# Kernel optimization log

Hardware: AMD Instinct MI355X
Metric: run time of the kernel (lower is better)

The kernel has to match this reference:

```python
import jax, jax.numpy as jnp
import numpy as np

B, N = 16, 286
EMB_DIM = 4
CLOUD_DIM = 4
NB = 3          # number_of_basis
HID = 150       # radial MLP hidden width
RADIUS = 3.0    # neighbor radius / max_radius of cosine basis
FF = 512


def sp5(x):
    # torch Softplus(beta=5)
    return jax.nn.softplus(5.0 * x) / 5.0


def cosine_basis(r):
    # e3nn CosineBasisModel embedding: cos^2 bumps on [0, RADIUS]
    centers = jnp.linspace(0.0, RADIUS, NB)
    step = centers[1] - centers[0]
    d = (r[..., None] - centers) / step                     # [B,N,N,NB]
    return jnp.cos(jnp.pi / 2 * d) ** 2 * (jnp.abs(d) < 1.0)


def cloud_conv(feats, dist, mask, ws, bs, dim_out):
    # radial MLP on pairwise distances -> per-pair [dim_out, dim_in] kernel (l=0 only)
    x = cosine_basis(dist)
    for w, b in zip(ws[:-1], bs[:-1]):
        x = sp5(x @ w + b)
    R = x @ ws[-1] + bs[-1]                                 # [B,N,N,dim_out*dim_in]
    b_, n_ = dist.shape[0], dist.shape[1]
    k = R.reshape(b_, n_, n_, dim_out, -1) * mask[..., None, None]
    nb = jnp.maximum(mask.sum(-1), 1.0)                     # neighbors per atom [B,N]
    out = jnp.einsum('zabij,zbj->zai', k, feats) / jnp.sqrt(nb)[..., None]
    return out


def setup_inputs() -> dict:
    key = jax.random.key(0)
    ks = jax.random.split(key, 32)
    xyz = jax.random.normal(ks[0], (B, N, 3), dtype=jnp.float32)
    Z = jax.random.randint(ks[1], (B, N), 0, 11)
    emb = jax.random.normal(ks[2], (11, EMB_DIM), dtype=jnp.float32)
    inp = {'xyz': xyz, 'Z': Z, 'emb': emb}
    # radial MLPs per cloud: 3 -> 150 -> 150 -> 150 -> dim_out*dim_in (=16)
    dims = [NB, HID, HID, HID, CLOUD_DIM * CLOUD_DIM]
    ki = 3
    for c in range(2):
        for l in range(4):
            w = jax.random.normal(ks[ki], (dims[l], dims[l + 1]), dtype=jnp.float32) / np.sqrt(dims[l])
            b = jnp.zeros((dims[l + 1],), dtype=jnp.float32)
            inp[f'c{c}_w{l}'] = w
            inp[f'c{c}_b{l}'] = b
            ki += 1
    cloud_out = CLOUD_DIM * 2  # cloud_dim * cloud_order^2 * nclouds = 8
    inp['fc_w'] = jax.random.normal(ks[ki], (cloud_out, FF), dtype=jnp.float32) / np.sqrt(cloud_out); ki += 1
    inp['fc_b'] = jnp.zeros((FF,), dtype=jnp.float32)
    inp['bn_g'] = jnp.ones((FF,), dtype=jnp.float32)
    inp['bn_b'] = jnp.zeros((FF,), dtype=jnp.float32)
    inp['out_w'] = jax.random.normal(ks[ki], (FF, 1), dtype=jnp.float32) / np.sqrt(FF); ki += 1
    inp['out_b'] = jnp.zeros((1,), dtype=jnp.float32)
    return inp


def reference(xyz, Z, emb,
              c0_w0, c0_b0, c0_w1, c0_b1, c0_w2, c0_b2, c0_w3, c0_b3,
              c1_w0, c1_b0, c1_w1, c1_b1, c1_w2, c1_b2, c1_w3, c1_b3,
              fc_w, fc_b, bn_g, bn_b, out_w, out_b):
    feats = emb[Z]                                          # [B,N,emb_dim]
    diff = xyz[:, :, None, :] - xyz[:, None, :, :]
    dist = jnp.sqrt(jnp.sum(diff * diff, -1) + 1e-12)       # [B,N,N]
    mask = (dist < RADIUS).astype(feats.dtype)
    f1 = cloud_conv(feats, dist, mask,
                    [c0_w0, c0_w1, c0_w2, c0_w3], [c0_b0, c0_b1, c0_b2, c0_b3], CLOUD_DIM)
    f2 = cloud_conv(f1, dist, mask,
                    [c1_w0, c1_w1, c1_w2, c1_w3], [c1_b0, c1_b1, c1_b2, c1_b3], CLOUD_DIM)
    feats_cat = jnp.concatenate([f1, f2], axis=2)           # [B,N,8]
    # lp_pool2d(norm=2, kernel=(N,1)) == L2 norm over atom dim
    pooled = jnp.sqrt(jnp.sum(feats_cat ** 2, axis=1))      # [B,8]
    h = jax.nn.softplus(pooled @ fc_w + fc_b)
    mean = h.mean(0)
    var = h.var(0)
    h = jax.nn.softplus((h - mean) / jnp.sqrt(var + 1e-5) * bn_g + bn_b)
    return jax.nn.sigmoid(h @ out_w + out_b)[:, 0]          # [B]
```

## Files before the change

### kernel.cpp

```cpp
#include <hip/hip_runtime.h>
#include <hip/hip_bf16.h>
#include <hip/hip_fp16.h>
#include <math.h>

#define B_SZ   16
#define N_ATOM 286
#define NT     1024
#define HIDW   150
#define FF_DIM 512
#define WPAD   152
#define WROWS  151

__device__ __forceinline__ float softplus_f(float x) {
  return fmaxf(x, 0.0f) + log1pf(expf(-fabsf(x)));
}
__device__ __forceinline__ float sp5_f(float x) {
  float t = 5.0f * x;
  return (fmaxf(t, 0.0f) + log1pf(expf(-fabsf(t)))) * 0.2f;
}

__global__ __launch_bounds__(256) void prep_kernel(
    const float* __restrict__ w1a, const float* __restrict__ b1a,
    const float* __restrict__ w2a, const float* __restrict__ b2a,
    const float* __restrict__ w1c, const float* __restrict__ b1c,
    const float* __restrict__ w2c, const float* __restrict__ b2c,
    float* __restrict__ Wp) {
  const int m = blockIdx.y;
  const float* W  = (m == 0) ? w1a : (m == 1) ? w2a : (m == 2) ? w1c : w2c;
  const float* Bb = (m == 0) ? b1a : (m == 1) ? b2a : (m == 2) ? b1c : b2c;
  int idx = blockIdx.x * 256 + threadIdx.x;
  if (idx < WROWS * WPAD) {
    int i = idx / WPAD, o = idx % WPAD;
    float v = 0.0f;
    if (o < HIDW) v = (i < HIDW) ? W[i * HIDW + o] : Bb[o];
    Wp[(size_t)m * WROWS * WPAD + idx] = v;
  }
}

__device__ __forceinline__ void hidden_layer_v2(
    const float* __restrict__ Wp,
    const float* __restrict__ src,
    float* __restrict__ dst,
    int jj, int e0) {
  const float4 bb = *(const float4*)(Wp + HIDW * WPAD + 4 * jj);
  float4 a0 = bb, a1 = bb;
  #pragma unroll 8
  for (int i = 0; i < HIDW; ++i) {
    float4 wv = *(const float4*)(Wp + i * WPAD + 4 * jj);
    float2 h  = *(const float2*)(src + i * 8 + e0);
    a0.x = __builtin_fmaf(h.x, wv.x, a0.x); a1.x = __builtin_fmaf(h.y, wv.x, a1.x);
    a0.y = __builtin_fmaf(h.x, wv.y, a0.y); a1.y = __builtin_fmaf(h.y, wv.y, a1.y);
    a0.z = __builtin_fmaf(h.x, wv.z, a0.z); a1.z = __builtin_fmaf(h.y, wv.z, a1.z);
    a0.w = __builtin_fmaf(h.x, wv.w, a0.w); a1.w = __builtin_fmaf(h.y, wv.w, a1.w);
  }
  *(float2*)(dst + (4 * jj + 0) * 8 + e0) = make_float2(sp5_f(a0.x), sp5_f(a1.x));
  *(float2*)(dst + (4 * jj + 1) * 8 + e0) = make_float2(sp5_f(a0.y), sp5_f(a1.y));
  *(float2*)(dst + (4 * jj + 2) * 8 + e0) = make_float2(sp5_f(a0.z), sp5_f(a1.z));
  *(float2*)(dst + (4 * jj + 3) * 8 + e0) = make_float2(sp5_f(a0.w), sp5_f(a1.w));
}

__global__ __launch_bounds__(256) void table_kernel(
    const float* __restrict__ a_w0, const float* __restrict__ a_b0,
    const float* __restrict__ a_w3, const float* __restrict__ a_b3,
    const float* __restrict__ c_w0, const float* __restrict__ c_b0,
    const float* __restrict__ c_w3, const float* __restrict__ c_b3,
    const float* __restrict__ Wp,
    __half* __restrict__ tabh0, __half* __restrict__ tabh1) {
  __shared__ float actA[WPAD * 8];
  __shared__ float actB[WPAD * 8];

  const int nblk = NT / 8;
  const int cloud = (blockIdx.x >= nblk) ? 1 : 0;
  const int blk   = blockIdx.x - cloud * nblk;
  const float* w0 = cloud ? c_w0 : a_w0;  const float* b0 = cloud ? c_b0 : a_b0;
  const float* w3 = cloud ? c_w3 : a_w3;  const float* b3 = cloud ? c_b3 : a_b3;
  const float* Wp1 = Wp + (size_t)(cloud * 2)     * WROWS * WPAD;
  const float* Wp2 = Wp + (size_t)(cloud * 2 + 1) * WROWS * WPAD;
  __half* table = cloud ? tabh1 : tabh0;

  const int tid  = threadIdx.x;
  const int lane = tid & 63;
  const int wave = __builtin_amdgcn_readfirstlane(tid >> 6);
  const int e0   = wave * 2;
  const int gbase = blk * 8;
  const int jj = (lane < 38) ? lane : 37;

  float x0[3], x1[3];
  #pragma unroll
  for (int k = 0; k < 3; ++k) {
    float r0 = 3.0f * (float)(gbase + e0)     / (float)(NT - 1);
    float r1 = 3.0f * (float)(gbase + e0 + 1) / (float)(NT - 1);
    float d0 = (r0 - 1.5f * (float)k) * (1.0f / 1.5f);
    float d1 = (r1 - 1.5f * (float)k) * (1.0f / 1.5f);
    float c0 = cosf(1.57079632679489662f * d0);
    float c1 = cosf(1.57079632679489662f * d1);
    x0[k] = (fabsf(d0) < 1.0f) ? c0 * c0 : 0.0f;
    x1[k] = (fabsf(d1) < 1.0f) ? c1 * c1 : 0.0f;
  }

  #pragma unroll
  for (int c = 0; c < 3; ++c) {
    int o = lane + 64 * c;
    int oc = (o < HIDW) ? o : (HIDW - 1);
    float w00 = w0[oc], w01 = w0[HIDW + oc], w02 = w0[2 * HIDW + oc], bb = b0[oc];
    float h0 = sp5_f(bb + x0[0] * w00 + x0[1] * w01 + x0[2] * w02);
    float h1 = sp5_f(bb + x1[0] * w00 + x1[1] * w01 + x1[2] * w02);
    if (o < HIDW) *(float2*)(actA + o * 8 + e0) = make_float2(h0, h1);
  }

  hidden_layer_v2(Wp1, actA, actB, jj, e0);
  hidden_layer_v2(Wp2, actB, actA, jj, e0);

  {
    const int o  = lane & 15;
    const int ig = lane >> 4;
    float a0 = 0.f, a1 = 0.f;
    for (int i = ig; i < HIDW; i += 4) {
      float wv = w3[i * 16 + o];
      float h0 = actA[i * 8 + e0];
      float h1 = actA[i * 8 + e0 + 1];
      a0 = __builtin_fmaf(h0, wv, a0);
      a1 = __builtin_fmaf(h1, wv, a1);
    }
    a0 += __shfl_xor(a0, 16, 64); a0 += __shfl_xor(a0, 32, 64);
    a1 += __shfl_xor(a1, 16, 64); a1 += __shfl_xor(a1, 32, 64);
    if (lane < 16) {
      float bb = b3[o];
      table[(size_t)(gbase + e0)     * 16 + o] = __float2half(a0 + bb);
      table[(size_t)(gbase + e0 + 1) * 16 + o] = __float2half(a1 + bb);
    }
  }
}

__device__ __forceinline__ void cvt8(uint4 q, float* out) {
  const __half2* h = (const __half2*)&q;
  #pragma unroll
  for (int k = 0; k < 4; ++k) {
    float2 f = __half22float2(h[k]);
    out[2 * k] = f.x; out[2 * k + 1] = f.y;
  }
}

__global__ __launch_bounds__(256) void conv_kernel(
    const float* __restrict__ xyz, const int* __restrict__ Z,
    const float* __restrict__ emb, const float* __restrict__ feats_in,
    const __half* __restrict__ tabh, float* __restrict__ f_out, int gather) {
  const int wave = threadIdx.x >> 6;
  const int lane = threadIdx.x & 63;
  const int row = blockIdx.x * 4 + wave;
  if (row >= B_SZ * N_ATOM) return;
  const int z = row / N_ATOM, a = row % N_ATOM;
  const float* xz = xyz + (size_t)z * N_ATOM * 3;
  const float ax = xz[a * 3 + 0], ay = xz[a * 3 + 1], az = xz[a * 3 + 2];

  float acc[4] = {0.f, 0.f, 0.f, 0.f};
  float cnt = 0.f;
  for (int b = lane; b < N_ATOM; b += 64) {
    float bx = xz[b * 3 + 0], by = xz[b * 3 + 1], bz = xz[b * 3 + 2];
    float dx = ax - bx, dy = ay - by, dz = az - bz;
    float r = sqrtf(dx * dx + dy * dy + dz * dz + 1e-12f);
    if (r < 3.0f) {
      cnt += 1.0f;
      float t = r * ((float)(NT - 1) / 3.0f);
      int idx = (int)t;
      if (idx > NT - 2) idx = NT - 2;
      float fr = t - (float)idx;
      const uint4* Tp = (const uint4*)(tabh + (size_t)idx * 16);
      uint4 q0 = Tp[0], q1 = Tp[1], q2 = Tp[2], q3 = Tp[3];
      float4 fb;
      if (gather) {
        int zi = Z[z * N_ATOM + b];
        fb = *(const float4*)(emb + (size_t)zi * 4);
      } else {
        fb = *(const float4*)(feats_in + ((size_t)z * N_ATOM + b) * 4);
      }
      float r0[16], r1[16];
      cvt8(q0, r0); cvt8(q1, r0 + 8);
      cvt8(q2, r1); cvt8(q3, r1 + 8);
      #pragma unroll
      for (int i = 0; i < 4; ++i) {
        float v0 = r0[4 * i + 0] + fr * (r1[4 * i + 0] - r0[4 * i + 0]);
        float v1 = r0[4 * i + 1] + fr * (r1[4 * i + 1] - r0[4 * i + 1]);
        float v2 = r0[4 * i + 2] + fr * (r1[4 * i + 2] - r0[4 * i + 2]);
        float v3 = r0[4 * i + 3] + fr * (r1[4 * i + 3] - r0[4 * i + 3]);
        acc[i] += v0 * fb.x + v1 * fb.y + v2 * fb.z + v3 * fb.w;
      }
    }
  }
  #pragma unroll
  for (int m = 32; m > 0; m >>= 1) {
    #pragma unroll
    for (int i = 0; i < 4; ++i) acc[i] += __shfl_xor(acc[i], m, 64);
    cnt += __shfl_xor(cnt, m, 64);
  }
  if (lane == 0) {
    float nb = cnt < 1.0f ? 1.0f : cnt;
    float sc = 1.0f / sqrtf(nb);
    float4 o;
    o.x = acc[0] * sc; o.y = acc[1] * sc; o.z = acc[2] * sc; o.w = acc[3] * sc;
    *(float4*)(f_out + (size_t)row * 4) = o;
  }
}

__global__ __launch_bounds__(256) void pool_kernel(
    const float* __restrict__ f1, const float* __restrict__ f2,
    float* __restrict__ pool_sq) {
  __shared__ float red[4][8];
  const int z = blockIdx.x;
  const int tid = threadIdx.x;
  const int lane = tid & 63, wave = tid >> 6;
  float s[8] = {0.f, 0.f, 0.f, 0.f, 0.f, 0.f, 0.f, 0.f};
  for (int a = tid; a < N_ATOM; a += 256) {
    float4 v1 = *(const float4*)(f1 + ((size_t)z * N_ATOM + a) * 4);
    float4 v2 = *(const float4*)(f2 + ((size_t)z * N_ATOM + a) * 4);
    s[0] += v1.x * v1.x; s[1] += v1.y * v1.y;
    s[2] += v1.z * v1.z; s[3] += v1.w * v1.w;
    s[4] += v2.x * v2.x; s[5] += v2.y * v2.y;
    s[6] += v2.z * v2.z; s[7] += v2.w * v2.w;
  }
  #pragma unroll
  for (int m = 32; m > 0; m >>= 1) {
    #pragma unroll
    for (int k = 0; k < 8; ++k) s[k] += __shfl_xor(s[k], m, 64);
  }
  if (lane == 0) {
    #pragma unroll
    for (int k = 0; k < 8; ++k) red[wave][k] = s[k];
  }
  __syncthreads();
  if (tid < 8)
    pool_sq[z * 8 + tid] = red[0][tid] + red[1][tid] + red[2][tid] + red[3][tid];
}

__global__ __launch_bounds__(512) void tail_kernel(
    const float* __restrict__ pool_sq,
    const float* __restrict__ fc_w, const float* __restrict__ fc_b,
    const float* __restrict__ bn_g, const float* __restrict__ bn_b,
    const float* __restrict__ out_w, const float* __restrict__ out_b,
    float* __restrict__ out) {
  __shared__ float pooled[16][8];
  __shared__ float part[8][16];
  const int tid = threadIdx.x;

  if (tid < 128) pooled[tid >> 3][tid & 7] = sqrtf(pool_sq[tid]);
  __syncthreads();

  const int f = tid;
  float hv[16];
  float mean = 0.f;
  #pragma unroll
  for (int z = 0; z < 16; ++z) {
    float a = fc_b[f];
    #pragma unroll
    for (int c = 0; c < 8; ++c) a += pooled[z][c] * fc_w[c * FF_DIM + f];
    hv[z] = softplus_f(a);
    mean += hv[z];
  }
  mean *= (1.0f / 16.0f);
  float var = 0.f;
  #pragma unroll
  for (int z = 0; z < 16; ++z) { float d = hv[z] - mean; var += d * d; }
  var *= (1.0f / 16.0f);
  float istd = 1.0f / sqrtf(var + 1e-5f);
  float g = bn_g[f], bb = bn_b[f], ow = out_w[f];
  float contrib[16];
  #pragma unroll
  for (int z = 0; z < 16; ++z)
    contrib[z] = softplus_f((hv[z] - mean) * istd * g + bb) * ow;

  const int lane = tid & 63, wv = tid >> 6;
  #pragma unroll
  for (int m = 32; m > 0; m >>= 1) {
    #pragma unroll
    for (int z = 0; z < 16; ++z) contrib[z] += __shfl_xor(contrib[z], m, 64);
  }
  if (lane == 0) {
    #pragma unroll
    for (int z = 0; z < 16; ++z) part[wv][z] = contrib[z];
  }
  __syncthreads();
  if (tid < 16) {
    float s = out_b[0];
    #pragma unroll
    for (int w8 = 0; w8 < 8; ++w8) s += part[w8][tid];
    out[tid] = 1.0f / (1.0f + expf(-s));
  }
}

extern "C" void kernel_launch(void* const* d_in, const int* in_sizes, int n_in,
                              void* d_out, int out_size, void* d_ws, size_t ws_size,
                              hipStream_t stream) {
  const float* xyz = (const float*)d_in[0];
  const int*   Z   = (const int*)d_in[1];
  const float* emb = (const float*)d_in[2];
  const float* c0[8]; const float* c1[8];
  for (int i = 0; i < 8; ++i) {
    c0[i] = (const float*)d_in[3 + i];
    c1[i] = (const float*)d_in[11 + i];
  }
  const float* fc_w  = (const float*)d_in[19];
  const float* fc_b  = (const float*)d_in[20];
  const float* bn_g  = (const float*)d_in[21];
  const float* bn_b  = (const float*)d_in[22];
  const float* out_w = (const float*)d_in[23];
  const float* out_b = (const float*)d_in[24];
  float* out = (float*)d_out;

  float* wsf = (float*)d_ws;
  float* Wp = wsf;
  float* f1 = Wp + (size_t)4 * WROWS * WPAD;
  float* f2 = f1 + (size_t)B_SZ * N_ATOM * 4;
  float* pool_sq = f2 + (size_t)B_SZ * N_ATOM * 4;
  __half* tabh0 = (__half*)(pool_sq + 128);
  __half* tabh1 = tabh0 + (size_t)NT * 16;

  {
    dim3 g((WROWS * WPAD + 255) / 256, 4);
    prep_kernel<<<g, 256, 0, stream>>>(c0[2], c0[3], c0[4], c0[5],
                                       c1[2], c1[3], c1[4], c1[5], Wp);
  }

  table_kernel<<<2 * (NT / 8), 256, 0, stream>>>(
      c0[0], c0[1], c0[6], c0[7],
      c1[0], c1[1], c1[6], c1[7],
      Wp, tabh0, tabh1);

  const int conv_blocks = (B_SZ * N_ATOM + 3) / 4;
  conv_kernel<<<conv_blocks, 256, 0, stream>>>(xyz, Z, emb, (const float*)nullptr,
                                               tabh0, f1, 1);
  conv_kernel<<<conv_blocks, 256, 0, stream>>>(xyz, Z, emb, f1,
                                               tabh1, f2, 0);

  pool_kernel<<<B_SZ, 256, 0, stream>>>(f1, f2, pool_sq);

  tail_kernel<<<1, 512, 0, stream>>>(pool_sq, fc_w, fc_b, bn_g, bn_b,
                                     out_w, out_b, out);
}
```

Baseline: 183.6 us.

## Stage per-molecule coordinates and features in LDS; branchless masked conv accumulation

Conv blocks are now assigned per molecule (72 blocks per batch element), and each block loads that molecule's coordinates and neighbor features into shared memory once. The per-pair loop reads positions and features from LDS instead of global memory. The radius test becomes a multiplicative mask, so table lookups run for every pair without divergence. The table kernel inlines the hidden-layer routine with restrict pointers and unroll 10. The cost is extra table loads for out-of-radius pairs and an added block-level sync.

```diff
diff --git a/kernel.cpp b/kernel.cpp
--- a/kernel.cpp
+++ b/kernel.cpp
@@ -10,6 +10,7 @@
 #define FF_DIM 512
 #define WPAD   152
 #define WROWS  151
+#define BLK_PER_Z 72
 
 __device__ __forceinline__ float softplus_f(float x) {
   return fmaxf(x, 0.0f) + log1pf(expf(-fabsf(x)));
@@ -37,28 +38,6 @@
   }
 }
 
-__device__ __forceinline__ void hidden_layer_v2(
-    const float* __restrict__ Wp,
-    const float* __restrict__ src,
-    float* __restrict__ dst,
-    int jj, int e0) {
-  const float4 bb = *(const float4*)(Wp + HIDW * WPAD + 4 * jj);
-  float4 a0 = bb, a1 = bb;
-  #pragma unroll 8
-  for (int i = 0; i < HIDW; ++i) {
-    float4 wv = *(const float4*)(Wp + i * WPAD + 4 * jj);
-    float2 h  = *(const float2*)(src + i * 8 + e0);
-    a0.x = __builtin_fmaf(h.x, wv.x, a0.x); a1.x = __builtin_fmaf(h.y, wv.x, a1.x);
-    a0.y = __builtin_fmaf(h.x, wv.y, a0.y); a1.y = __builtin_fmaf(h.y, wv.y, a1.y);
-    a0.z = __builtin_fmaf(h.x, wv.z, a0.z); a1.z = __builtin_fmaf(h.y, wv.z, a1.z);
-    a0.w = __builtin_fmaf(h.x, wv.w, a0.w); a1.w = __builtin_fmaf(h.y, wv.w, a1.w);
-  }
-  *(float2*)(dst + (4 * jj + 0) * 8 + e0) = make_float2(sp5_f(a0.x), sp5_f(a1.x));
-  *(float2*)(dst + (4 * jj + 1) * 8 + e0) = make_float2(sp5_f(a0.y), sp5_f(a1.y));
-  *(float2*)(dst + (4 * jj + 2) * 8 + e0) = make_float2(sp5_f(a0.z), sp5_f(a1.z));
-  *(float2*)(dst + (4 * jj + 3) * 8 + e0) = make_float2(sp5_f(a0.w), sp5_f(a1.w));
-}
-
 __global__ __launch_bounds__(256) void table_kernel(
     const float* __restrict__ a_w0, const float* __restrict__ a_b0,
     const float* __restrict__ a_w3, const float* __restrict__ a_b3,
@@ -74,8 +53,8 @@
   const int blk   = blockIdx.x - cloud * nblk;
   const float* w0 = cloud ? c_w0 : a_w0;  const float* b0 = cloud ? c_b0 : a_b0;
   const float* w3 = cloud ? c_w3 : a_w3;  const float* b3 = cloud ? c_b3 : a_b3;
-  const float* Wp1 = Wp + (size_t)(cloud * 2)     * WROWS * WPAD;
-  const float* Wp2 = Wp + (size_t)(cloud * 2 + 1) * WROWS * WPAD;
+  const float* __restrict__ Wp1 = Wp + (size_t)(cloud * 2)     * WROWS * WPAD;
+  const float* __restrict__ Wp2 = Wp + (size_t)(cloud * 2 + 1) * WROWS * WPAD;
   __half* table = cloud ? tabh1 : tabh0;
 
   const int tid  = threadIdx.x;
@@ -105,11 +84,46 @@
     float w00 = w0[oc], w01 = w0[HIDW + oc], w02 = w0[2 * HIDW + oc], bb = b0[oc];
     float h0 = sp5_f(bb + x0[0] * w00 + x0[1] * w01 + x0[2] * w02);
     float h1 = sp5_f(bb + x1[0] * w00 + x1[1] * w01 + x1[2] * w02);
-    if (o < HIDW) *(float2*)(actA + o * 8 + e0) = make_float2(h0, h1);
-  }
-
-  hidden_layer_v2(Wp1, actA, actB, jj, e0);
-  hidden_layer_v2(Wp2, actB, actA, jj, e0);
+    if (o < HIDW) *(float2*)(&actA[o * 8 + e0]) = make_float2(h0, h1);
+  }
+
+  {
+    const float* __restrict__ Wb = Wp1 + 4 * jj;
+    float4 a0 = *(const float4*)(Wp1 + HIDW * WPAD + 4 * jj);
+    float4 a1 = a0;
+    #pragma unroll 10
+    for (int i = 0; i < HIDW; ++i) {
+      float4 wv = *(const float4*)(Wb + i * WPAD);
+      float2 h  = *(const float2*)(&actA[i * 8 + e0]);
+      a0.x = __builtin_fmaf(h.x, wv.x, a0.x); a1.x = __builtin_fmaf(h.y, wv.x, a1.x);
+      a0.y = __builtin_fmaf(h.x, wv.y, a0.y); a1.y = __builtin_fmaf(h.y, wv.y, a1.y);
+      a0.z = __builtin_fmaf(h.x, wv.z, a0.z); a1.z = __builtin_fmaf(h.y, wv.z, a1.z);
+      a0.w = __builtin_fmaf(h.x, wv.w, a0.w); a1.w = __builtin_fmaf(h.y, wv.w, a1.w);
+    }
+    *(float2*)(&actB[(4 * jj + 0) * 8 + e0]) = make_float2(sp5_f(a0.x), sp5_f(a1.x));
+    *(float2*)(&actB[(4 * jj + 1) * 8 + e0]) = make_float2(sp5_f(a0.y), sp5_f(a1.y));
+    *(float2*)(&actB[(4 * jj + 2) * 8 + e0]) = make_float2(sp5_f(a0.z), sp5_f(a1.z));
+    *(float2*)(&actB[(4 * jj + 3) * 8 + e0]) = make_float2(sp5_f(a0.w), sp5_f(a1.w));
+  }
+
+  {
+    const float* __restrict__ Wb = Wp2 + 4 * jj;
+    float4 a0 = *(const float4*)(Wp2 + HIDW * WPAD + 4 * jj);
+    float4 a1 = a0;
+    #pragma unroll 10
+    for (int i = 0; i < HIDW; ++i) {
+      float4 wv = *(const float4*)(Wb + i * WPAD);
+      float2 h  = *(const float2*)(&actB[i * 8 + e0]);
+      a0.x = __builtin_fmaf(h.x, wv.x, a0.x); a1.x = __builtin_fmaf(h.y, wv.x, a1.x);
+      a0.y = __builtin_fmaf(h.x, wv.y, a0.y); a1.y = __builtin_fmaf(h.y, wv.y, a1.y);
+      a0.z = __builtin_fmaf(h.x, wv.z, a0.z); a1.z = __builtin_fmaf(h.y, wv.z, a1.z);
+      a0.w = __builtin_fmaf(h.x, wv.w, a0.w); a1.w = __builtin_fmaf(h.y, wv.w, a1.w);
+    }
+    *(float2*)(&actA[(4 * jj + 0) * 8 + e0]) = make_float2(sp5_f(a0.x), sp5_f(a1.x));
+    *(float2*)(&actA[(4 * jj + 1) * 8 + e0]) = make_float2(sp5_f(a0.y), sp5_f(a1.y));
+    *(float2*)(&actA[(4 * jj + 2) * 8 + e0]) = make_float2(sp5_f(a0.z), sp5_f(a1.z));
+    *(float2*)(&actA[(4 * jj + 3) * 8 + e0]) = make_float2(sp5_f(a0.w), sp5_f(a1.w));
+  }
 
   {
     const int o  = lane & 15;
@@ -145,46 +159,56 @@
     const float* __restrict__ xyz, const int* __restrict__ Z,
     const float* __restrict__ emb, const float* __restrict__ feats_in,
     const __half* __restrict__ tabh, float* __restrict__ f_out, int gather) {
-  const int wave = threadIdx.x >> 6;
-  const int lane = threadIdx.x & 63;
-  const int row = blockIdx.x * 4 + wave;
-  if (row >= B_SZ * N_ATOM) return;
-  const int z = row / N_ATOM, a = row % N_ATOM;
-  const float* xz = xyz + (size_t)z * N_ATOM * 3;
-  const float ax = xz[a * 3 + 0], ay = xz[a * 3 + 1], az = xz[a * 3 + 2];
+  __shared__ float xs[N_ATOM], ys[N_ATOM], zs[N_ATOM];
+  __shared__ float fxs[N_ATOM], fys[N_ATOM], fzs[N_ATOM], fws[N_ATOM];
+  const int tid  = threadIdx.x;
+  const int wave = tid >> 6;
+  const int lane = tid & 63;
+  const int z = blockIdx.x / BLK_PER_Z;
+  const int a = (blockIdx.x % BLK_PER_Z) * 4 + wave;
+
+  for (int b = tid; b < N_ATOM; b += 256) {
+    const float* p = xyz + ((size_t)z * N_ATOM + b) * 3;
+    xs[b] = p[0]; ys[b] = p[1]; zs[b] = p[2];
+    float4 fb;
+    if (gather) {
+      int zi = Z[z * N_ATOM + b];
+      fb = *(const float4*)(emb + (size_t)zi * 4);
+    } else {
+      fb = *(const float4*)(feats_in + ((size_t)z * N_ATOM + b) * 4);
+    }
+    fxs[b] = fb.x; fys[b] = fb.y; fzs[b] = fb.z; fws[b] = fb.w;
+  }
+  __syncthreads();
+  if (a >= N_ATOM) return;
+
+  const float ax = xs[a], ay = ys[a], az = zs[a];
 
   float acc[4] = {0.f, 0.f, 0.f, 0.f};
   float cnt = 0.f;
   for (int b = lane; b < N_ATOM; b += 64) {
-    float bx = xz[b * 3 + 0], by = xz[b * 3 + 1], bz = xz[b * 3 + 2];
-    float dx = ax - bx, dy = ay - by, dz = az - bz;
+    float dx = ax - xs[b], dy = ay - ys[b], dz = az - zs[b];
     float r = sqrtf(dx * dx + dy * dy + dz * dz + 1e-12f);
-    if (r < 3.0f) {
-      cnt += 1.0f;
-      float t = r * ((float)(NT - 1) / 3.0f);
-      int idx = (int)t;
-      if (idx > NT - 2) idx = NT - 2;
-      float fr = t - (float)idx;
-      const uint4* Tp = (const uint4*)(tabh + (size_t)idx * 16);
-      uint4 q0 = Tp[0], q1 = Tp[1], q2 = Tp[2], q3 = Tp[3];
-      float4 fb;
-      if (gather) {
-        int zi = Z[z * N_ATOM + b];
-        fb = *(const float4*)(emb + (size_t)zi * 4);
-      } else {
-        fb = *(const float4*)(feats_in + ((size_t)z * N_ATOM + b) * 4);
-      }
-      float r0[16], r1[16];
-      cvt8(q0, r0); cvt8(q1, r0 + 8);
-      cvt8(q2, r1); cvt8(q3, r1 + 8);
-      #pragma unroll
-      for (int i = 0; i < 4; ++i) {
-        float v0 = r0[4 * i + 0] + fr * (r1[4 * i + 0] - r0[4 * i + 0]);
-        float v1 = r0[4 * i + 1] + fr * (r1[4 * i + 1] - r0[4 * i + 1]);
-        float v2 = r0[4 * i + 2] + fr * (r1[4 * i + 2] - r0[4 * i + 2]);
-        float v3 = r0[4 * i + 3] + fr * (r1[4 * i + 3] - r0[4 * i + 3]);
-        acc[i] += v0 * fb.x + v1 * fb.y + v2 * fb.z + v3 * fb.w;
-      }
+    float msk = (r < 3.0f) ? 1.0f : 0.0f;
+    float t = r * ((float)(NT - 1) / 3.0f);
+    int idx = (int)t;
+    if (idx > NT - 2) idx = NT - 2;
+    float fr = t - (float)idx;
+    const uint4* Tp = (const uint4*)(tabh + (size_t)idx * 16);
+    uint4 q0 = Tp[0], q1 = Tp[1], q2 = Tp[2], q3 = Tp[3];
+    float fbx = fxs[b], fby = fys[b], fbz = fzs[b], fbw = fws[b];
+    cnt += msk;
+    float r0[16], r1[16];
+    cvt8(q0, r0); cvt8(q1, r0 + 8);
+    cvt8(q2, r1); cvt8(q3, r1 + 8);
+    #pragma unroll
+    for (int i = 0; i < 4; ++i) {
+      float v0 = r0[4 * i + 0] + fr * (r1[4 * i + 0] - r0[4 * i + 0]);
+      float v1 = r0[4 * i + 1] + fr * (r1[4 * i + 1] - r0[4 * i + 1]);
+      float v2 = r0[4 * i + 2] + fr * (r1[4 * i + 2] - r0[4 * i + 2]);
+      float v3 = r0[4 * i + 3] + fr * (r1[4 * i + 3] - r0[4 * i + 3]);
+      acc[i] = __builtin_fmaf(msk, v0 * fbx + v1 * fby + v2 * fbz + v3 * fbw,
+                              acc[i]);
     }
   }
   #pragma unroll
@@ -198,7 +222,7 @@
     float sc = 1.0f / sqrtf(nb);
     float4 o;
     o.x = acc[0] * sc; o.y = acc[1] * sc; o.z = acc[2] * sc; o.w = acc[3] * sc;
-    *(float4*)(f_out + (size_t)row * 4) = o;
+    *(float4*)(f_out + ((size_t)z * N_ATOM + a) * 4) = o;
   }
 }
 
@@ -325,7 +349,7 @@
       c1[0], c1[1], c1[6], c1[7],
       Wp, tabh0, tabh1);
 
-  const int conv_blocks = (B_SZ * N_ATOM + 3) / 4;
+  const int conv_blocks = B_SZ * BLK_PER_Z;
   conv_kernel<<<conv_blocks, 256, 0, stream>>>(xyz, Z, emb, (const float*)nullptr,
                                                tabh0, f1, 1);
   conv_kernel<<<conv_blocks, 256, 0, stream>>>(xyz, Z, emb, f1,
```

Result: no change. 180.1 us (-1.9%).
